# Optimization experiments

Hardware: AMD Instinct MI355X
Metric: run time of the kernel (lower is better)

Reference implementation:

```python
import jax, jax.numpy as jnp
import numpy as np
from jax import lax

N_PTS = 500000
CH = 64
GRID = 256
BN_EPS = 1e-5
A = -0.75  # torch bicubic coefficient


def setup_inputs() -> dict:
    key = jax.random.key(0)
    ks = jax.random.split(key, 10)
    coordinates = jax.random.uniform(ks[0], (N_PTS, 3), jnp.float32) * 2.0 - 1.0  # points in [-1,1]^3
    noise = jax.random.normal(ks[1], (3, N_PTS, 2), jnp.float32) * 0.01  # per-plane coord jitter (is_training)
    plane_x = jax.random.normal(ks[2], (1, CH, GRID, GRID), jnp.float32) * 0.001
    plane_y = jax.random.normal(ks[3], (1, CH, GRID, GRID), jnp.float32) * 0.001
    plane_z = jax.random.normal(ks[4], (1, CH, GRID, GRID), jnp.float32) * 0.001
    fan_in = CH * 9
    conv_w = jax.random.uniform(ks[5], (CH, CH, 3, 3), jnp.float32, -1.0, 1.0) / np.sqrt(fan_in)
    conv_b = jax.random.uniform(ks[6], (CH,), jnp.float32, -1.0, 1.0) / np.sqrt(fan_in)
    bn_gamma = jnp.ones((CH,), jnp.float32)
    bn_beta = jnp.zeros((CH,), jnp.float32)
    return {"coordinates": coordinates, "noise": noise, "plane_x": plane_x,
            "plane_y": plane_y, "plane_z": plane_z, "conv_w": conv_w,
            "conv_b": conv_b, "bn_gamma": bn_gamma, "bn_beta": bn_beta}


def res_block(p, conv_w, conv_b, gamma, beta):
    # conv3x3 stride2 pad1 -> BN (batch stats, training mode) -> relu, + avgpool3x3 s2 p1 (count_include_pad)
    y = lax.conv_general_dilated(p, conv_w, (2, 2), [(1, 1), (1, 1)],
                                 dimension_numbers=("NCHW", "OIHW", "NCHW"))
    y = y + conv_b[None, :, None, None]
    mu = jnp.mean(y, axis=(0, 2, 3), keepdims=True)
    var = jnp.var(y, axis=(0, 2, 3), keepdims=True)  # biased, as torch BN uses for normalization
    y = (y - mu) * lax.rsqrt(var + BN_EPS) * gamma[None, :, None, None] + beta[None, :, None, None]
    y = jax.nn.relu(y)
    pooled = lax.reduce_window(p, 0.0, lax.add, (1, 1, 3, 3), (1, 1, 2, 2),
                               [(0, 0), (0, 0), (1, 1), (1, 1)]) / 9.0
    return y + pooled


def cubic_weights(t):
    # torch cubic convolution weights, a=-0.75; t in [0,1). returns (4, M)
    t1 = t + 1.0
    w0 = ((A * t1 - 5 * A) * t1 + 8 * A) * t1 - 4 * A
    w1 = ((A + 2) * t - (A + 3)) * t * t + 1.0
    s = 1.0 - t
    w2 = ((A + 2) * s - (A + 3)) * s * s + 1.0
    w3 = 1.0 - w0 - w1 - w2
    return jnp.stack([w0, w1, w2, w3])


def sample_plane_bicubic(plane, grid):
    # plane: (C,H,W); grid: (M,2) with grid[:,0]->W axis, grid[:,1]->H axis (torch grid_sample layout)
    # bicubic, padding_mode='border', align_corners=True
    C, H, W = plane.shape
    gx = jnp.clip((grid[:, 0] + 1.0) * 0.5 * (W - 1), 0.0, W - 1.0)
    gy = jnp.clip((grid[:, 1] + 1.0) * 0.5 * (H - 1), 0.0, H - 1.0)
    x0f = jnp.floor(gx); y0f = jnp.floor(gy)
    tx = gx - x0f; ty = gy - y0f
    x0 = x0f.astype(jnp.int32); y0 = y0f.astype(jnp.int32)
    wx = cubic_weights(tx)  # (4,M)
    wy = cubic_weights(ty)  # (4,M)
    pl = jnp.transpose(plane, (1, 2, 0))  # (H,W,C)
    out = jnp.zeros((grid.shape[0], C), plane.dtype)
    for i in range(4):  # fixed 4x4 bicubic footprint
        yi = jnp.clip(y0 + (i - 1), 0, H - 1)
        for j in range(4):
            xi = jnp.clip(x0 + (j - 1), 0, W - 1)
            out = out + (wy[i] * wx[j])[:, None] * pl[yi, xi]
    return out  # (M,C)


def reference(coordinates, noise, plane_x, plane_y, plane_z, conv_w, conv_b, bn_gamma, bn_beta):
    bound = 1.0
    c = (coordinates + bound) / (2.0 * bound)  # (N,3) in [0,1] (fed to grid_sample as-is, faithful)
    px = res_block(plane_x, conv_w, conv_b, bn_gamma, bn_beta)[0]  # (C,128,128)
    py = res_block(plane_y, conv_w, conv_b, bn_gamma, bn_beta)[0]
    pz = res_block(plane_z, conv_w, conv_b, bn_gamma, bn_beta)[0]
    xy = sample_plane_bicubic(px, c[:, 0:2] + noise[0])
    yz = sample_plane_bicubic(py, c[:, 1:3] + noise[1])
    xz = sample_plane_bicubic(pz, c[:, 0:3:2] + noise[2])
    return xy + yz + xz  # (N,C)
```

## Files before the change

kernel.cpp:

```cpp
#include <hip/hip_runtime.h>
#include <hip/hip_fp16.h>

#define N_POINTS 500000
#define BN_EPS 1e-5f
#define A_COEF -0.75f

typedef __attribute__((ext_vector_type(8))) short short8;
typedef __attribute__((ext_vector_type(4))) float floatx4;
typedef unsigned short ushort_t;
typedef unsigned int uint_t;

#define WS_WBF_OFF    0
#define WS_CONV_OFF   18432
#define WS_SUM_OFF    (WS_CONV_OFF + 3145728)
#define WS_SUMSQ_OFF  (WS_SUM_OFF + 192)
#define WS_SCALE_OFF  (WS_SUMSQ_OFF + 192)
#define WS_SHIFT_OFF  (WS_SCALE_OFF + 192)
#define WS_PLANES_OFF (WS_SHIFT_OFF + 192)
#define WS_INBF_OFF   (WS_PLANES_OFF + 1572864)
#define WS_REC_OFF    WS_INBF_OFF
#define WS_BIN_OFF    (WS_INBF_OFF + 6291456)

__device__ __forceinline__ ushort_t f2bf(float f) {
  uint_t u = __float_as_uint(f);
  uint_t r = (u + 0x7fffu + ((u >> 16) & 1u)) >> 16;
  return (ushort_t)r;
}
__device__ __forceinline__ float bf2f(ushort_t u) {
  return __uint_as_float(((uint_t)u) << 16);
}
__device__ __forceinline__ int cell_of(float c0, float c1, float c2) {
  int q0 = min(15, max(0, (int)(c0 * 16.0f)));
  int q1 = min(15, max(0, (int)(c1 * 16.0f)));
  int q2 = min(15, max(0, (int)(c2 * 16.0f)));
  return (q0 << 8) | (q1 << 4) | q2;
}

__global__ __launch_bounds__(256) void wprep_kernel(const float* __restrict__ w_in,
                                                    float* __restrict__ ws) {
  int i = blockIdx.x * 256 + threadIdx.x;
  if (i < 36864) {
    int ic = i & 63;
    int oc = (i >> 6) & 63;
    int kk = i >> 12;
    ((ushort_t*)(ws + WS_WBF_OFF))[i] = f2bf(w_in[(oc * 64 + ic) * 9 + kk]);
  }
  if (i < 384) ws[WS_SUM_OFF + i] = 0.0f;
  if (i < 8192) ((int*)(ws + WS_BIN_OFF))[i] = 0;
}

__global__ __launch_bounds__(256) void hist_kernel(const float* __restrict__ coords,
                                                   float* __restrict__ ws) {
  int n = blockIdx.x * 256 + threadIdx.x;
  if (n >= N_POINTS) return;
  float c0 = (coords[n * 3 + 0] + 1.0f) * 0.5f;
  float c1 = (coords[n * 3 + 1] + 1.0f) * 0.5f;
  float c2 = (coords[n * 3 + 2] + 1.0f) * 0.5f;
  atomicAdd(&((int*)(ws + WS_BIN_OFF))[cell_of(c0, c1, c2)], 1);
}

__global__ __launch_bounds__(256) void scan_kernel(float* __restrict__ ws) {
  __shared__ int sums[256];
  int* hist = (int*)(ws + WS_BIN_OFF);
  int* offs = hist + 4096;
  int t = threadIdx.x;
  int local[16], s = 0;
#pragma unroll
  for (int k = 0; k < 16; k++) { local[k] = hist[t * 16 + k]; s += local[k]; }
  sums[t] = s;
  __syncthreads();
  for (int d = 1; d < 256; d <<= 1) {
    int v = (t >= d) ? sums[t - d] : 0;
    __syncthreads();
    sums[t] += v;
    __syncthreads();
  }
  int excl = sums[t] - s;
#pragma unroll
  for (int k = 0; k < 16; k++) { offs[t * 16 + k] = excl; excl += local[k]; }
}

__global__ __launch_bounds__(256) void scatter_kernel(const float* __restrict__ coords,
                                                      const float* __restrict__ noise,
                                                      float* __restrict__ ws) {
  int n = blockIdx.x * 256 + threadIdx.x;
  if (n >= N_POINTS) return;
  float c0 = (coords[n * 3 + 0] + 1.0f) * 0.5f;
  float c1 = (coords[n * 3 + 1] + 1.0f) * 0.5f;
  float c2 = (coords[n * 3 + 2] + 1.0f) * 0.5f;
  int cell = cell_of(c0, c1, c2);
  int* offs = (int*)(ws + WS_BIN_OFF) + 4096;
  int pos = atomicAdd(&offs[cell], 1);
  float u0 = c0 + noise[(0 * N_POINTS + n) * 2 + 0];
  float v0 = c1 + noise[(0 * N_POINTS + n) * 2 + 1];
  float u1 = c1 + noise[(1 * N_POINTS + n) * 2 + 0];
  float v1 = c2 + noise[(1 * N_POINTS + n) * 2 + 1];
  float u2 = c0 + noise[(2 * N_POINTS + n) * 2 + 0];
  float v2 = c2 + noise[(2 * N_POINTS + n) * 2 + 1];
  float4* rec = (float4*)(ws + WS_REC_OFF) + pos * 2;
  rec[0] = make_float4(u0, v0, u1, v1);
  rec[1] = make_float4(u2, v2, __int_as_float(n), 0.0f);
}

__global__ __launch_bounds__(256) void transpose_kernel(const float* __restrict__ p0,
                                                        const float* __restrict__ p1,
                                                        const float* __restrict__ p2,
                                                        float* __restrict__ ws) {
  __shared__ float tile[64][65];
  const int xt = blockIdx.x, y = blockIdx.y, pl = blockIdx.z;
  const float* src = (pl == 0) ? p0 : ((pl == 1) ? p1 : p2);
  ushort_t* dst = (ushort_t*)(ws + WS_INBF_OFF) + pl * (256 * 256 * 64);
  const int t = threadIdx.x;
  const int x0 = xt * 64;
  for (int i = t; i < 4096; i += 256) {
    int c = i >> 6, x = i & 63;
    tile[x][c] = src[(c * 256 + y) * 256 + x0 + x];
  }
  __syncthreads();
  uint_t* du = (uint_t*)dst;
  for (int i = t; i < 2048; i += 256) {
    int x = i >> 5, cp = (i & 31) * 2;
    uint_t lo = f2bf(tile[x][cp]);
    uint_t hi = f2bf(tile[x][cp + 1]);
    du[((y * 256 + x0 + x) * 64 + cp) >> 1] = (hi << 16) | lo;
  }
}

__global__ __launch_bounds__(256) void conv_mfma_kernel(const float* __restrict__ ws_r,
                                                        float* __restrict__ ws) {
  const int xh = blockIdx.x, oy = blockIdx.y, pz = blockIdx.z;
  const int t = threadIdx.x;
  const int wv = t >> 6, lane = t & 63;
  const int mn = lane & 15;
  const int kg = lane >> 4;
  const int x0w = xh * 64 + wv * 16;

  const ushort_t* inb = (const ushort_t*)(ws_r + WS_INBF_OFF) + pz * (256 * 256 * 64);
  const ushort_t* wbf = (const ushort_t*)(ws_r + WS_WBF_OFF);

  floatx4 acc[4] = {{0.f,0.f,0.f,0.f},{0.f,0.f,0.f,0.f},{0.f,0.f,0.f,0.f},{0.f,0.f,0.f,0.f}};

  for (int ky = 0; ky < 3; ky++) {
    int y = 2 * oy - 1 + ky;
    if (y < 0) continue;
    const ushort_t* rowp = inb + y * (256 * 64);
    for (int kx = 0; kx < 3; kx++) {
      int xm = 2 * (x0w + mn) - 1 + kx;
      bool vx = xm >= 0;
      int xc = vx ? xm : 0;
      const ushort_t* abase = rowp + xc * 64 + kg * 8;
      const ushort_t* wbase = wbf + ((ky * 3 + kx) * 64 + mn) * 64 + kg * 8;
#pragma unroll
      for (int kc = 0; kc < 2; kc++) {
        union { int4 i4; short8 s8; } au;
        au.i4 = *reinterpret_cast<const int4*>(abase + kc * 32);
        if (!vx) au.i4 = make_int4(0, 0, 0, 0);
#pragma unroll
        for (int nt = 0; nt < 4; nt++) {
          union { int4 i4; short8 s8; } bu;
          bu.i4 = *reinterpret_cast<const int4*>(wbase + nt * 1024 + kc * 32);
          acc[nt] = __builtin_amdgcn_mfma_f32_16x16x32_bf16(au.s8, bu.s8, acc[nt], 0, 0, 0);
        }
      }
    }
  }
  float* cout = ws + WS_CONV_OFF + ((pz * 128 + oy) * 128 + x0w) * 64;
#pragma unroll
  for (int nt = 0; nt < 4; nt++) {
#pragma unroll
    for (int r = 0; r < 4; r++) {
      cout[(kg * 4 + r) * 64 + nt * 16 + mn] = acc[nt][r];
    }
  }
}

__global__ __launch_bounds__(256) void stats_kernel(float* __restrict__ ws) {
  const int b = blockIdx.x;
  const int plane = b >> 6, chunk = b & 63;
  const int t = threadIdx.x;
  const int c = t & 63, g = t >> 6;
  const float* base = ws + WS_CONV_OFF + plane * (16384 * 64);
  float s = 0.0f, s2 = 0.0f;
  const int row0 = chunk * 256 + g * 64;
  for (int i = 0; i < 64; i++) {
    float v = base[(row0 + i) * 64 + c];
    s += v;
    s2 = fmaf(v, v, s2);
  }
  __shared__ float rs[256], rs2[256];
  rs[t] = s; rs2[t] = s2;
  __syncthreads();
  if (t < 64) {
    s = rs[t] + rs[t + 64] + rs[t + 128] + rs[t + 192];
    s2 = rs2[t] + rs2[t + 64] + rs2[t + 128] + rs2[t + 192];
    atomicAdd(&ws[WS_SUM_OFF + plane * 64 + c], s);
    atomicAdd(&ws[WS_SUMSQ_OFF + plane * 64 + c], s2);
  }
}

__global__ void finalize_kernel(const float* __restrict__ gamma,
                                const float* __restrict__ beta,
                                float* __restrict__ ws) {
  int i = threadIdx.x;
  if (i < 192) {
    int c = i & 63;
    float mu = ws[WS_SUM_OFF + i] * (1.0f / 16384.0f);
    float var = ws[WS_SUMSQ_OFF + i] * (1.0f / 16384.0f) - mu * mu;
    var = fmaxf(var, 0.0f);
    float rstd = 1.0f / sqrtf(var + BN_EPS);
    float sc = gamma[c] * rstd;
    ws[WS_SCALE_OFF + i] = sc;
    ws[WS_SHIFT_OFF + i] = beta[c] - mu * sc;
  }
}

__global__ __launch_bounds__(256) void apply_kernel(float* __restrict__ ws,
                                                    __half* __restrict__ planes) {
  int idx = blockIdx.x * 256 + threadIdx.x;
  int g = idx & 7;
  int p = (idx >> 3) & 16383;
  int pl = idx >> 17;
  int oy = p >> 7, ox = p & 127;
  int cb = g * 8;

  const float* conv = ws + WS_CONV_OFF;
  float4 a0 = *reinterpret_cast<const float4*>(conv + (size_t)idx * 8);
  float4 a1 = *reinterpret_cast<const float4*>(conv + (size_t)idx * 8 + 4);

  float sc[8], sh[8];
#pragma unroll
  for (int k = 0; k < 8; k++) {
    sc[k] = ws[WS_SCALE_OFF + pl * 64 + cb + k];
    sh[k] = ws[WS_SHIFT_OFF + pl * 64 + cb + k];
  }

  const ushort_t* inb = (const ushort_t*)(ws + WS_INBF_OFF) + pl * (256 * 256 * 64);
  float ps[8];
#pragma unroll
  for (int k = 0; k < 8; k++) ps[k] = 0.0f;
#pragma unroll
  for (int r = 0; r < 3; r++) {
    int yy = 2 * oy - 1 + r;
    if (yy < 0) continue;
#pragma unroll
    for (int s = 0; s < 3; s++) {
      int xx = 2 * ox - 1 + s;
      if (xx < 0) continue;
      union { int4 i4; ushort_t u[8]; } ub;
      ub.i4 = *reinterpret_cast<const int4*>(inb + (yy * 256 + xx) * 64 + cb);
#pragma unroll
      for (int k = 0; k < 8; k++) ps[k] += bf2f(ub.u[k]);
    }
  }

  float v[8] = {a0.x, a0.y, a0.z, a0.w, a1.x, a1.y, a1.z, a1.w};
  union { int4 i4; __half h[8]; } ob;
#pragma unroll
  for (int k = 0; k < 8; k++) {
    float r = fmaxf(fmaf(v[k], sc[k], sh[k]), 0.0f) + ps[k] * (1.0f / 9.0f);
    ob.h[k] = __float2half(r);
  }
  *reinterpret_cast<int4*>(planes + (size_t)idx * 8) = ob.i4;
}

__device__ __forceinline__ void cubic_w(float t, float w[4]) {
  float t1 = t + 1.0f;
  w[0] = ((A_COEF * t1 - 5.0f * A_COEF) * t1 + 8.0f * A_COEF) * t1 - 4.0f * A_COEF;
  w[1] = ((A_COEF + 2.0f) * t - (A_COEF + 3.0f)) * t * t + 1.0f;
  float s = 1.0f - t;
  w[2] = ((A_COEF + 2.0f) * s - (A_COEF + 3.0f)) * s * s + 1.0f;
  w[3] = 1.0f - w[0] - w[1] - w[2];
}

__global__ __launch_bounds__(256) void sample_kernel(const float* __restrict__ ws,
                                                     const __half* __restrict__ planes,
                                                     float* __restrict__ out) {
  const int t = threadIdx.x;
  const int wv = t >> 6, lane = t & 63;
  const int g = lane >> 3, l = lane & 7;
  const int idx = blockIdx.x * 32 + wv * 8 + g;

  const float4* rec = (const float4*)(ws + WS_REC_OFF) + (size_t)idx * 2;
  float4 r0 = rec[0];
  float4 r1 = rec[1];
  const int n = __float_as_int(r1.z);
  float uu[3] = {r0.x, r0.z, r1.x};
  float vv[3] = {r0.y, r0.w, r1.y};

  float acc[8];
#pragma unroll
  for (int e = 0; e < 8; e++) acc[e] = 0.0f;

  const char* pbase = (const char*)planes + l * 16;

#pragma unroll
  for (int p = 0; p < 3; p++) {
    float gx = fminf(fmaxf(fmaf(uu[p], 63.5f, 63.5f), 0.0f), 127.0f);
    float gy = fminf(fmaxf(fmaf(vv[p], 63.5f, 63.5f), 0.0f), 127.0f);
    float x0f = floorf(gx), y0f = floorf(gy);
    float tx = gx - x0f, ty = gy - y0f;
    int ix = (int)x0f, iy = (int)y0f;
    float wx[4], wy[4];
    cubic_w(tx, wx);
    cubic_w(ty, wy);
    uint_t yo[4], xo[4];
#pragma unroll
    for (int i = 0; i < 4; i++) yo[i] = (uint_t)min(max(iy - 1 + i, 0), 127) * 16384u;
#pragma unroll
    for (int j = 0; j < 4; j++) xo[j] = (uint_t)min(max(ix - 1 + j, 0), 127) * 128u;
    const char* pb = pbase + (size_t)p * 2097152;
#pragma unroll
    for (int i = 0; i < 4; i++) {
      const char* rp = pb + yo[i];
#pragma unroll
      for (int j = 0; j < 4; j++) {
        union { int4 i4; __half h[8]; } ub;
        ub.i4 = *reinterpret_cast<const int4*>(rp + xo[j]);
        float w = wy[i] * wx[j];
#pragma unroll
        for (int q = 0; q < 8; q++) {
          acc[q] = fmaf(__half2float(ub.h[q]), w, acc[q]);
        }
      }
    }
  }
  float4* op = reinterpret_cast<float4*>(out + (size_t)n * 64 + l * 8);
  op[0] = make_float4(acc[0], acc[1], acc[2], acc[3]);
  op[1] = make_float4(acc[4], acc[5], acc[6], acc[7]);
}

extern "C" void kernel_launch(void* const* d_in, const int* in_sizes, int n_in,
                              void* d_out, int out_size, void* d_ws, size_t ws_size,
                              hipStream_t stream) {
  const float* coords = (const float*)d_in[0];
  const float* noise  = (const float*)d_in[1];
  const float* px     = (const float*)d_in[2];
  const float* py     = (const float*)d_in[3];
  const float* pz     = (const float*)d_in[4];
  const float* conv_w = (const float*)d_in[5];
  const float* gamma  = (const float*)d_in[7];
  const float* beta   = (const float*)d_in[8];
  float* out = (float*)d_out;
  float* ws = (float*)d_ws;
  __half* planes = (__half*)(ws + WS_PLANES_OFF);

  wprep_kernel<<<144, 256, 0, stream>>>(conv_w, ws);
  hist_kernel<<<1954, 256, 0, stream>>>(coords, ws);
  scan_kernel<<<1, 256, 0, stream>>>(ws);
  transpose_kernel<<<dim3(4, 256, 3), 256, 0, stream>>>(px, py, pz, ws);
  conv_mfma_kernel<<<dim3(2, 128, 3), 256, 0, stream>>>(ws, ws);
  stats_kernel<<<192, 256, 0, stream>>>(ws);
  finalize_kernel<<<1, 256, 0, stream>>>(gamma, beta, ws);
  apply_kernel<<<1536, 256, 0, stream>>>(ws, planes);
  scatter_kernel<<<1954, 256, 0, stream>>>(coords, noise, ws);
  sample_kernel<<<15625, 256, 0, stream>>>(ws, planes, out);
}
```

Measured before the change: 414.2 us.

## Fuse prep kernels, fold BN stats into conv, use half2 FMA in sampler

Merges weight prep, histogram and transpose into one launch, and computes the BN sums inside the conv epilogue, which removes the separate stats pass over the conv output. The scan and finalize steps are combined into one kernel. The conv weights are laid out per lane so each B-fragment load is contiguous. The sampler now accumulates each row of the bicubic footprint with packed half2 FMAs before scaling by the row weight in fp32, which halves the FMA count but adds fp16 rounding error. The workspace offsets are reorganised and zeroing is done with a memset.

```diff
diff --git a/kernel.cpp b/kernel.cpp
--- a/kernel.cpp
+++ b/kernel.cpp
@@ -12,14 +12,15 @@
 
 #define WS_WBF_OFF    0
 #define WS_CONV_OFF   18432
-#define WS_SUM_OFF    (WS_CONV_OFF + 3145728)
-#define WS_SUMSQ_OFF  (WS_SUM_OFF + 192)
-#define WS_SCALE_OFF  (WS_SUMSQ_OFF + 192)
-#define WS_SHIFT_OFF  (WS_SCALE_OFF + 192)
-#define WS_PLANES_OFF (WS_SHIFT_OFF + 192)
+#define WS_PLANES_OFF (WS_CONV_OFF + 3145728)
 #define WS_INBF_OFF   (WS_PLANES_OFF + 1572864)
 #define WS_REC_OFF    WS_INBF_OFF
-#define WS_BIN_OFF    (WS_INBF_OFF + 6291456)
+#define WS_SUM_OFF    (WS_INBF_OFF + 6291456)
+#define WS_SUMSQ_OFF  (WS_SUM_OFF + 192)
+#define WS_HIST_OFF   (WS_SUMSQ_OFF + 192)
+#define WS_OFFS_OFF   (WS_HIST_OFF + 4096)
+#define WS_SCALE_OFF  (WS_OFFS_OFF + 4096)
+#define WS_SHIFT_OFF  (WS_SCALE_OFF + 192)
 
 __device__ __forceinline__ ushort_t f2bf(float f) {
   uint_t u = __float_as_uint(f);
@@ -36,33 +37,125 @@
   return (q0 << 8) | (q1 << 4) | q2;
 }
 
-__global__ __launch_bounds__(256) void wprep_kernel(const float* __restrict__ w_in,
-                                                    float* __restrict__ ws) {
-  int i = blockIdx.x * 256 + threadIdx.x;
-  if (i < 36864) {
-    int ic = i & 63;
-    int oc = (i >> 6) & 63;
-    int kk = i >> 12;
-    ((ushort_t*)(ws + WS_WBF_OFF))[i] = f2bf(w_in[(oc * 64 + ic) * 9 + kk]);
-  }
-  if (i < 384) ws[WS_SUM_OFF + i] = 0.0f;
-  if (i < 8192) ((int*)(ws + WS_BIN_OFF))[i] = 0;
-}
-
-__global__ __launch_bounds__(256) void hist_kernel(const float* __restrict__ coords,
+__global__ __launch_bounds__(256) void prep_kernel(const float* __restrict__ p0,
+                                                   const float* __restrict__ p1,
+                                                   const float* __restrict__ p2,
+                                                   const float* __restrict__ w_in,
+                                                   const float* __restrict__ coords,
                                                    float* __restrict__ ws) {
-  int n = blockIdx.x * 256 + threadIdx.x;
-  if (n >= N_POINTS) return;
-  float c0 = (coords[n * 3 + 0] + 1.0f) * 0.5f;
-  float c1 = (coords[n * 3 + 1] + 1.0f) * 0.5f;
-  float c2 = (coords[n * 3 + 2] + 1.0f) * 0.5f;
-  atomicAdd(&((int*)(ws + WS_BIN_OFF))[cell_of(c0, c1, c2)], 1);
-}
-
-__global__ __launch_bounds__(256) void scan_kernel(float* __restrict__ ws) {
+  __shared__ float tile[64][65];
+  const int xt = blockIdx.x, y = blockIdx.y, pl = blockIdx.z;
+  const int bid = (pl * 256 + y) * 4 + xt;
+  const int t = threadIdx.x;
+
+  if (bid < 1954) {
+    int n = bid * 256 + t;
+    if (n < N_POINTS) {
+      float c0 = (coords[n * 3 + 0] + 1.0f) * 0.5f;
+      float c1 = (coords[n * 3 + 1] + 1.0f) * 0.5f;
+      float c2 = (coords[n * 3 + 2] + 1.0f) * 0.5f;
+      atomicAdd(&((int*)(ws + WS_HIST_OFF))[cell_of(c0, c1, c2)], 1);
+    }
+  }
+  if (bid >= 2048 && bid < 2192) {
+    int i = (bid - 2048) * 256 + t;
+    int j = i & 7;
+    int lane = (i >> 3) & 63;
+    int nt = (i >> 9) & 3;
+    int kc = (i >> 11) & 1;
+    int tap = i >> 12;
+    int oc = nt * 16 + (lane & 15);
+    int ic = kc * 32 + (lane >> 4) * 8 + j;
+    ((ushort_t*)(ws + WS_WBF_OFF))[i] = f2bf(w_in[(oc * 64 + ic) * 9 + tap]);
+  }
+
+  const float* src = (pl == 0) ? p0 : ((pl == 1) ? p1 : p2);
+  ushort_t* dst = (ushort_t*)(ws + WS_INBF_OFF) + pl * (256 * 256 * 64);
+  const int x0 = xt * 64;
+  for (int i = t; i < 4096; i += 256) {
+    int c = i >> 6, x = i & 63;
+    tile[x][c] = src[(c * 256 + y) * 256 + x0 + x];
+  }
+  __syncthreads();
+  uint_t* du = (uint_t*)dst;
+  for (int i = t; i < 2048; i += 256) {
+    int x = i >> 5, cp = (i & 31) * 2;
+    uint_t lo = f2bf(tile[x][cp]);
+    uint_t hi = f2bf(tile[x][cp + 1]);
+    du[((y * 256 + x0 + x) * 64 + cp) >> 1] = (hi << 16) | lo;
+  }
+}
+
+__global__ __launch_bounds__(256) void conv_mfma_kernel(const float* __restrict__ ws_r,
+                                                        float* __restrict__ ws) {
+  __shared__ float reds[16][64];
+  __shared__ float redq[16][64];
+  const int xh = blockIdx.x, oy = blockIdx.y, pz = blockIdx.z;
+  const int t = threadIdx.x;
+  const int wv = t >> 6, lane = t & 63;
+  const int mn = lane & 15;
+  const int kg = lane >> 4;
+  const int x0w = xh * 64 + wv * 16;
+
+  const ushort_t* inb = (const ushort_t*)(ws_r + WS_INBF_OFF) + pz * (256 * 256 * 64);
+  const ushort_t* wbf = (const ushort_t*)(ws_r + WS_WBF_OFF);
+
+  floatx4 acc[4] = {{0.f,0.f,0.f,0.f},{0.f,0.f,0.f,0.f},{0.f,0.f,0.f,0.f},{0.f,0.f,0.f,0.f}};
+
+  for (int ky = 0; ky < 3; ky++) {
+    int y = 2 * oy - 1 + ky;
+    if (y < 0) continue;
+    const ushort_t* rowp = inb + y * (256 * 64);
+    for (int kx = 0; kx < 3; kx++) {
+      int xm = 2 * (x0w + mn) - 1 + kx;
+      bool vx = xm >= 0;
+      int xc = vx ? xm : 0;
+      const ushort_t* abase = rowp + xc * 64 + kg * 8;
+      const int tap = ky * 3 + kx;
+#pragma unroll
+      for (int kc = 0; kc < 2; kc++) {
+        union { int4 i4; short8 s8; } au;
+        au.i4 = *reinterpret_cast<const int4*>(abase + kc * 32);
+        if (!vx) au.i4 = make_int4(0, 0, 0, 0);
+#pragma unroll
+        for (int nt = 0; nt < 4; nt++) {
+          union { int4 i4; short8 s8; } bu;
+          bu.i4 = *reinterpret_cast<const int4*>(wbf + ((((tap * 2 + kc) * 4 + nt) * 64 + lane) << 3));
+          acc[nt] = __builtin_amdgcn_mfma_f32_16x16x32_bf16(au.s8, bu.s8, acc[nt], 0, 0, 0);
+        }
+      }
+    }
+  }
+  float* cout = ws + WS_CONV_OFF + ((pz * 128 + oy) * 128 + x0w) * 64;
+#pragma unroll
+  for (int nt = 0; nt < 4; nt++) {
+    float s = 0.0f, s2 = 0.0f;
+#pragma unroll
+    for (int r = 0; r < 4; r++) {
+      float v = acc[nt][r];
+      cout[(kg * 4 + r) * 64 + nt * 16 + mn] = v;
+      s += v;
+      s2 = fmaf(v, v, s2);
+    }
+    reds[wv * 4 + kg][nt * 16 + mn] = s;
+    redq[wv * 4 + kg][nt * 16 + mn] = s2;
+  }
+  __syncthreads();
+  if (t < 64) {
+    float s = 0.0f, s2 = 0.0f;
+#pragma unroll
+    for (int r = 0; r < 16; r++) { s += reds[r][t]; s2 += redq[r][t]; }
+    atomicAdd(&ws[WS_SUM_OFF + pz * 64 + t], s);
+    atomicAdd(&ws[WS_SUMSQ_OFF + pz * 64 + t], s2);
+  }
+}
+
+__global__ __launch_bounds__(256) void scanfin_kernel(const float* __restrict__ gamma,
+                                                      const float* __restrict__ beta,
+                                                      float* __restrict__ ws) {
   __shared__ int sums[256];
-  int* hist = (int*)(ws + WS_BIN_OFF);
-  int* offs = hist + 4096;
+  int* hist = (int*)(ws + WS_HIST_OFF);
+  int* offs = (int*)(ws + WS_OFFS_OFF);
   int t = threadIdx.x;
   int local[16], s = 0;
 #pragma unroll
@@ -78,6 +171,66 @@
   int excl = sums[t] - s;
 #pragma unroll
   for (int k = 0; k < 16; k++) { offs[t * 16 + k] = excl; excl += local[k]; }
+
+  if (t < 192) {
+    int c = t & 63;
+    float mu = ws[WS_SUM_OFF + t] * (1.0f / 16384.0f);
+    float var = ws[WS_SUMSQ_OFF + t] * (1.0f / 16384.0f) - mu * mu;
+    var = fmaxf(var, 0.0f);
+    float rstd = 1.0f / sqrtf(var + BN_EPS);
+    float sc = gamma[c] * rstd;
+    ws[WS_SCALE_OFF + t] = sc;
+    ws[WS_SHIFT_OFF + t] = beta[c] - mu * sc;
+  }
+}
+
+__global__ __launch_bounds__(256) void apply_kernel(float* __restrict__ ws,
+                                                    __half* __restrict__ planes) {
+  int idx = blockIdx.x * 256 + threadIdx.x;
+  int g = idx & 7;
+  int p = (idx >> 3) & 16383;
+  int pl = idx >> 17;
+  int oy = p >> 7, ox = p & 127;
+  int cb = g * 8;
+
+  const float* conv = ws + WS_CONV_OFF;
+  float4 a0 = *reinterpret_cast<const float4*>(conv + (size_t)idx * 8);
+  float4 a1 = *reinterpret_cast<const float4*>(conv + (size_t)idx * 8 + 4);
+
+  float sc[8], sh[8];
+#pragma unroll
+  for (int k = 0; k < 8; k++) {
+    sc[k] = ws[WS_SCALE_OFF + pl * 64 + cb + k];
+    sh[k] = ws[WS_SHIFT_OFF + pl * 64 + cb + k];
+  }
+
+  const ushort_t* inb = (const ushort_t*)(ws + WS_INBF_OFF) + pl * (256 * 256 * 64);
+  float ps[8];
+#pragma unroll
+  for (int k = 0; k < 8; k++) ps[k] = 0.0f;
+#pragma unroll
+  for (int r = 0; r < 3; r++) {
+    int yy = 2 * oy - 1 + r;
+    if (yy < 0) continue;
+#pragma unroll
+    for (int s = 0; s < 3; s++) {
+      int xx = 2 * ox - 1 + s;
+      if (xx < 0) continue;
+      union { int4 i4; ushort_t u[8]; } ub;
+      ub.i4 = *reinterpret_cast<const int4*>(inb + (yy * 256 + xx) * 64 + cb);
+#pragma unroll
+      for (int k = 0; k < 8; k++) ps[k] += bf2f(ub.u[k]);
+    }
+  }
+
+  float v[8] = {a0.x, a0.y, a0.z, a0.w, a1.x, a1.y, a1.z, a1.w};
+  union { int4 i4; __half h[8]; } ob;
+#pragma unroll
+  for (int k = 0; k < 8; k++) {
+    float r = fmaxf(fmaf(v[k], sc[k], sh[k]), 0.0f) + ps[k] * (1.0f / 9.0f);
+    ob.h[k] = __float2half(r);
+  }
+  *reinterpret_cast<int4*>(planes + (size_t)idx * 8) = ob.i4;
 }
 
 __global__ __launch_bounds__(256) void scatter_kernel(const float* __restrict__ coords,
@@ -89,8 +242,7 @@
   float c1 = (coords[n * 3 + 1] + 1.0f) * 0.5f;
   float c2 = (coords[n * 3 + 2] + 1.0f) * 0.5f;
   int cell = cell_of(c0, c1, c2);
-  int* offs = (int*)(ws + WS_BIN_OFF) + 4096;
-  int pos = atomicAdd(&offs[cell], 1);
+  int pos = atomicAdd(&((int*)(ws + WS_OFFS_OFF))[cell], 1);
   float u0 = c0 + noise[(0 * N_POINTS + n) * 2 + 0];
   float v0 = c1 + noise[(0 * N_POINTS + n) * 2 + 1];
   float u1 = c1 + noise[(1 * N_POINTS + n) * 2 + 0];
@@ -102,167 +254,6 @@
   rec[1] = make_float4(u2, v2, __int_as_float(n), 0.0f);
 }
 
-__global__ __launch_bounds__(256) void transpose_kernel(const float* __restrict__ p0,
-                                                        const float* __restrict__ p1,
-                                                        const float* __restrict__ p2,
-                                                        float* __restrict__ ws) {
-  __shared__ float tile[64][65];
-  const int xt = blockIdx.x, y = blockIdx.y, pl = blockIdx.z;
-  const float* src = (pl == 0) ? p0 : ((pl == 1) ? p1 : p2);
-  ushort_t* dst = (ushort_t*)(ws + WS_INBF_OFF) + pl * (256 * 256 * 64);
-  const int t = threadIdx.x;
-  const int x0 = xt * 64;
-  for (int i = t; i < 4096; i += 256) {
-    int c = i >> 6, x = i & 63;
-    tile[x][c] = src[(c * 256 + y) * 256 + x0 + x];
-  }
-  __syncthreads();
-  uint_t* du = (uint_t*)dst;
-  for (int i = t; i < 2048; i += 256) {
-    int x = i >> 5, cp = (i & 31) * 2;
-    uint_t lo = f2bf(tile[x][cp]);
-    uint_t hi = f2bf(tile[x][cp + 1]);
-    du[((y * 256 + x0 + x) * 64 + cp) >> 1] = (hi << 16) | lo;
-  }
-}
-
-__global__ __launch_bounds__(256) void conv_mfma_kernel(const float* __restrict__ ws_r,
-                                                        float* __restrict__ ws) {
-  const int xh = blockIdx.x, oy = blockIdx.y, pz = blockIdx.z;
-  const int t = threadIdx.x;
-  const int wv = t >> 6, lane = t & 63;
-  const int mn = lane & 15;
-  const int kg = lane >> 4;
-  const int x0w = xh * 64 + wv * 16;
-
-  const ushort_t* inb = (const ushort_t*)(ws_r + WS_INBF_OFF) + pz * (256 * 256 * 64);
-  const ushort_t* wbf = (const ushort_t*)(ws_r + WS_WBF_OFF);
-
-  floatx4 acc[4] = {{0.f,0.f,0.f,0.f},{0.f,0.f,0.f,0.f},{0.f,0.f,0.f,0.f},{0.f,0.f,0.f,0.f}};
-
-  for (int ky = 0; ky < 3; ky++) {
-    int y = 2 * oy - 1 + ky;
-    if (y < 0) continue;
-    const ushort_t* rowp = inb + y * (256 * 64);
-    for (int kx = 0; kx < 3; kx++) {
-      int xm = 2 * (x0w + mn) - 1 + kx;
-      bool vx = xm >= 0;
-      int xc = vx ? xm : 0;
-      const ushort_t* abase = rowp + xc * 64 + kg * 8;
-      const ushort_t* wbase = wbf + ((ky * 3 + kx) * 64 + mn) * 64 + kg * 8;
-#pragma unroll
-      for (int kc = 0; kc < 2; kc++) {
-        union { int4 i4; short8 s8; } au;
-        au.i4 = *reinterpret_cast<const int4*>(abase + kc * 32);
-        if (!vx) au.i4 = make_int4(0, 0, 0, 0);
-#pragma unroll
-        for (int nt = 0; nt < 4; nt++) {
-          union { int4 i4; short8 s8; } bu;
-          bu.i4 = *reinterpret_cast<const int4*>(wbase + nt * 1024 + kc * 32);
-          acc[nt] = __builtin_amdgcn_mfma_f32_16x16x32_bf16(au.s8, bu.s8, acc[nt], 0, 0, 0);
-        }
-      }
-    }
-  }
-  float* cout = ws + WS_CONV_OFF + ((pz * 128 + oy) * 128 + x0w) * 64;
-#pragma unroll
-  for (int nt = 0; nt < 4; nt++) {
-#pragma unroll
-    for (int r = 0; r < 4; r++) {
-      cout[(kg * 4 + r) * 64 + nt * 16 + mn] = acc[nt][r];
-    }
-  }
-}
-
-__global__ __launch_bounds__(256) void stats_kernel(float* __restrict__ ws) {
-  const int b = blockIdx.x;
-  const int plane = b >> 6, chunk = b & 63;
-  const int t = threadIdx.x;
-  const int c = t & 63, g = t >> 6;
-  const float* base = ws + WS_CONV_OFF + plane * (16384 * 64);
-  float s = 0.0f, s2 = 0.0f;
-  const int row0 = chunk * 256 + g * 64;
-  for (int i = 0; i < 64; i++) {
-    float v = base[(row0 + i) * 64 + c];
-    s += v;
-    s2 = fmaf(v, v, s2);
-  }
-  __shared__ float rs[256], rs2[256];
-  rs[t] = s; rs2[t] = s2;
-  __syncthreads();
-  if (t < 64) {
-    s = rs[t] + rs[t + 64] + rs[t + 128] + rs[t + 192];
-    s2 = rs2[t] + rs2[t + 64] + rs2[t + 128] + rs2[t + 192];
-    atomicAdd(&ws[WS_SUM_OFF + plane * 64 + c], s);
-    atomicAdd(&ws[WS_SUMSQ_OFF + plane * 64 + c], s2);
-  }
-}
-
-__global__ void finalize_kernel(const float* __restrict__ gamma,
-                                const float* __restrict__ beta,
-                                float* __restrict__ ws) {
-  int i = threadIdx.x;
-  if (i < 192) {
-    int c = i & 63;
-    float mu = ws[WS_SUM_OFF + i] * (1.0f / 16384.0f);
-    float var = ws[WS_SUMSQ_OFF + i] * (1.0f / 16384.0f) - mu * mu;
-    var = fmaxf(var, 0.0f);
-    float rstd = 1.0f / sqrtf(var + BN_EPS);
-    float sc = gamma[c] * rstd;
-    ws[WS_SCALE_OFF + i] = sc;
-    ws[WS_SHIFT_OFF + i] = beta[c] - mu * sc;
-  }
-}
-
-__global__ __launch_bounds__(256) void apply_kernel(float* __restrict__ ws,
-                                                    __half* __restrict__ planes) {
-  int idx = blockIdx.x * 256 + threadIdx.x;
-  int g = idx & 7;
-  int p = (idx >> 3) & 16383;
-  int pl = idx >> 17;
-  int oy = p >> 7, ox = p & 127;
-  int cb = g * 8;
-
-  const float* conv = ws + WS_CONV_OFF;
-  float4 a0 = *reinterpret_cast<const float4*>(conv + (size_t)idx * 8);
-  float4 a1 = *reinterpret_cast<const float4*>(conv + (size_t)idx * 8 + 4);
-
-  float sc[8], sh[8];
-#pragma unroll
-  for (int k = 0; k < 8; k++) {
-    sc[k] = ws[WS_SCALE_OFF + pl * 64 + cb + k];
-    sh[k] = ws[WS_SHIFT_OFF + pl * 64 + cb + k];
-  }
-
-  const ushort_t* inb = (const ushort_t*)(ws + WS_INBF_OFF) + pl * (256 * 256 * 64);
-  float ps[8];
-#pragma unroll
-  for (int k = 0; k < 8; k++) ps[k] = 0.0f;
-#pragma unroll
-  for (int r = 0; r < 3; r++) {
-    int yy = 2 * oy - 1 + r;
-    if (yy < 0) continue;
-#pragma unroll
-    for (int s = 0; s < 3; s++) {
-      int xx = 2 * ox - 1 + s;
-      if (xx < 0) continue;
-      union { int4 i4; ushort_t u[8]; } ub;
-      ub.i4 = *reinterpret_cast<const int4*>(inb + (yy * 256 + xx) * 64 + cb);
-#pragma unroll
-      for (int k = 0; k < 8; k++) ps[k] += bf2f(ub.u[k]);
-    }
-  }
-
-  float v[8] = {a0.x, a0.y, a0.z, a0.w, a1.x, a1.y, a1.z, a1.w};
-  union { int4 i4; __half h[8]; } ob;
-#pragma unroll
-  for (int k = 0; k < 8; k++) {
-    float r = fmaxf(fmaf(v[k], sc[k], sh[k]), 0.0f) + ps[k] * (1.0f / 9.0f);
-    ob.h[k] = __float2half(r);
-  }
-  *reinterpret_cast<int4*>(planes + (size_t)idx * 8) = ob.i4;
-}
-
 __device__ __forceinline__ void cubic_w(float t, float w[4]) {
   float t1 = t + 1.0f;
   w[0] = ((A_COEF * t1 - 5.0f * A_COEF) * t1 + 8.0f * A_COEF) * t1 - 4.0f * A_COEF;
@@ -287,9 +278,9 @@
   float uu[3] = {r0.x, r0.z, r1.x};
   float vv[3] = {r0.y, r0.w, r1.y};
 
-  float acc[8];
-#pragma unroll
-  for (int e = 0; e < 8; e++) acc[e] = 0.0f;
+  float facc[8];
+#pragma unroll
+  for (int e = 0; e < 8; e++) facc[e] = 0.0f;
 
   const char* pbase = (const char*)planes + l * 16;
 
@@ -308,25 +299,34 @@
     for (int i = 0; i < 4; i++) yo[i] = (uint_t)min(max(iy - 1 + i, 0), 127) * 16384u;
 #pragma unroll
     for (int j = 0; j < 4; j++) xo[j] = (uint_t)min(max(ix - 1 + j, 0), 127) * 128u;
+    __half2 wxh[4];
+#pragma unroll
+    for (int j = 0; j < 4; j++) wxh[j] = __float2half2_rn(wx[j]);
     const char* pb = pbase + (size_t)p * 2097152;
 #pragma unroll
     for (int i = 0; i < 4; i++) {
       const char* rp = pb + yo[i];
+      __half2 r2[4];
+#pragma unroll
+      for (int q = 0; q < 4; q++) r2[q] = __float2half2_rn(0.0f);
 #pragma unroll
       for (int j = 0; j < 4; j++) {
-        union { int4 i4; __half h[8]; } ub;
+        union { int4 i4; __half2 h2[4]; } ub;
         ub.i4 = *reinterpret_cast<const int4*>(rp + xo[j]);
-        float w = wy[i] * wx[j];
-#pragma unroll
-        for (int q = 0; q < 8; q++) {
-          acc[q] = fmaf(__half2float(ub.h[q]), w, acc[q]);
-        }
+#pragma unroll
+        for (int q = 0; q < 4; q++) r2[q] = __hfma2(ub.h2[q], wxh[j], r2[q]);
       }
+      float wyv = wy[i];
+#pragma unroll
+      for (int q = 0; q < 4; q++) {
+        facc[2 * q]     = fmaf(__low2float(r2[q]),  wyv, facc[2 * q]);
+        facc[2 * q + 1] = fmaf(__high2float(r2[q]), wyv, facc[2 * q + 1]);
+      }
     }
   }
   float4* op = reinterpret_cast<float4*>(out + (size_t)n * 64 + l * 8);
-  op[0] = make_float4(acc[0], acc[1], acc[2], acc[3]);
-  op[1] = make_float4(acc[4], acc[5], acc[6], acc[7]);
+  op[0] = make_float4(facc[0], facc[1], facc[2], facc[3]);
+  op[1] = make_float4(facc[4], facc[5], facc[6], facc[7]);
 }
 
 extern "C" void kernel_launch(void* const* d_in, const int* in_sizes, int n_in,
@@ -344,13 +344,10 @@
   float* ws = (float*)d_ws;
   __half* planes = (__half*)(ws + WS_PLANES_OFF);
 
-  wprep_kernel<<<144, 256, 0, stream>>>(conv_w, ws);
-  hist_kernel<<<1954, 256, 0, stream>>>(coords, ws);
-  scan_kernel<<<1, 256, 0, stream>>>(ws);
-  transpose_kernel<<<dim3(4, 256, 3), 256, 0, stream>>>(px, py, pz, ws);
+  hipMemsetAsync(ws + WS_SUM_OFF, 0, 8576 * sizeof(float), stream);
+  prep_kernel<<<dim3(4, 256, 3), 256, 0, stream>>>(px, py, pz, conv_w, coords, ws);
   conv_mfma_kernel<<<dim3(2, 128, 3), 256, 0, stream>>>(ws, ws);
-  stats_kernel<<<192, 256, 0, stream>>>(ws);
-  finalize_kernel<<<1, 256, 0, stream>>>(gamma, beta, ws);
+  scanfin_kernel<<<1, 256, 0, stream>>>(gamma, beta, ws);
   apply_kernel<<<1536, 256, 0, stream>>>(ws, planes);
   scatter_kernel<<<1954, 256, 0, stream>>>(coords, noise, ws);
   sample_kernel<<<15625, 256, 0, stream>>>(ws, planes, out);
```

Measured after the change: 392.7 us. -5.2%, faster.
